# Optimization experiments

Measured on AMD Instinct MI355X. Metric: run time of the kernel, lower is better.

## Reference

```python
import jax, jax.numpy as jnp
import numpy as np

P = 16  # patch size

def _transpose_mask(w, h):
    # torch loop: skip transpose iff j > W/3 and j < 2W/3 and k > H/3 and k < 2H/3
    jj = np.arange(w)
    kk = np.arange(h)
    inner_j = (jj > w / 3) & (jj < 2 * w / 3)
    inner_k = (kk > h / 3) & (kk < 2 * h / 3)
    keep = inner_j[:, None] & inner_k[None, :]        # (w, h) inner region, unchanged
    return jnp.asarray(~keep)                          # True -> transpose patch

def setup_inputs() -> dict:
    key = jax.random.key(0)
    x = jax.random.normal(key, (256, 3, 224, 224), dtype=jnp.float32)
    return {"x": x}

def reference(x):
    B, C, Hi, Wi = x.shape
    h, w = Hi // P, Wi // P
    # 'b c (h p1) (w p2) -> b w h p1 p2 c'
    xp = x.reshape(B, C, h, P, w, P).transpose(0, 4, 2, 3, 5, 1)  # (B, w, h, p1, p2, C)
    mask = _transpose_mask(w, h)                                    # (w, h)
    xt = jnp.swapaxes(xp, 3, 4)                                     # per-patch p1<->p2 transpose
    xo = jnp.where(mask[None, :, :, None, None, None], xt, xp)
    # 'b w h p2 p1 c -> b c (h p2) (w p1)'
    out = xo.transpose(0, 5, 2, 3, 1, 4).reshape(B, C, h * P, w * P)
    return out
```

## Files before the change

kernel.cpp:

```cpp
#include <hip/hip_runtime.h>


constexpr int PS = 16;
constexpr int LP = 17;

__global__ __launch_bounds__(256) void patch_rot_kernel(
    const float* __restrict__ in, float* __restrict__ out,
    int h, int w, int Wi) {
  __shared__ float lds[4][PS * LP];

  const int wave = threadIdx.x >> 6;
  const int lane = threadIdx.x & 63;
  const int pid  = blockIdx.x * 4 + wave;

  const int wj = pid % w;
  const int t1 = pid / w;
  const int hk = t1 % h;
  const int bc = t1 / h;

  const long plane = (long)bc * (long)(h * PS) * (long)Wi;

  const int i  = lane >> 2;
  const int j4 = (lane & 3) << 2;

  const long off = plane + (long)(hk * PS + i) * Wi + (long)(wj * PS + j4);

  const float4 v = *reinterpret_cast<const float4*>(in + off);

  const bool inner = (3 * wj > w) && (3 * wj < 2 * w) &&
                     (3 * hk > h) && (3 * hk < 2 * h);

  float* L = lds[wave];
  L[i * LP + j4 + 0] = v.x;
  L[i * LP + j4 + 1] = v.y;
  L[i * LP + j4 + 2] = v.z;
  L[i * LP + j4 + 3] = v.w;
  __syncthreads();

  float4 o;
  if (!inner) {
    o.x = L[(j4 + 0) * LP + i];
    o.y = L[(j4 + 1) * LP + i];
    o.z = L[(j4 + 2) * LP + i];
    o.w = L[(j4 + 3) * LP + i];
  } else {
    o = v;
  }

  *reinterpret_cast<float4*>(out + off) = o;
}

extern "C" void kernel_launch(void* const* d_in, const int* in_sizes, int n_in,
                              void* d_out, int out_size, void* d_ws, size_t ws_size,
                              hipStream_t stream) {
  const float* in = (const float*)d_in[0];
  float* out = (float*)d_out;

  const int B = 256, C = 3, Hi = 224, Wi = 224;
  const int h = Hi / PS;
  const int w = Wi / PS;

  const int npatch = B * C * h * w;
  const int nblocks = npatch / 4;

  patch_rot_kernel<<<nblocks, 256, 0, stream>>>(in, out, h, w, Wi);
}
```

Baseline: 58.30 us.

## Process four patches per wave and replace block barrier with LDS waitcnt

Measured after the change: 67.08 us. 1.15x slower.

```diff
diff --git a/kernel.cpp b/kernel.cpp
--- a/kernel.cpp
+++ b/kernel.cpp
@@ -1,53 +1,69 @@
 #include <hip/hip_runtime.h>
 
 
-constexpr int PS = 16;
-constexpr int LP = 17;
+constexpr int PS  = 16;
+constexpr int LP  = 17;
+constexpr int PPW = 4;
 
 __global__ __launch_bounds__(256) void patch_rot_kernel(
     const float* __restrict__ in, float* __restrict__ out,
     int h, int w, int Wi) {
-  __shared__ float lds[4][PS * LP];
+  __shared__ float lds[4][PPW][PS * LP];
 
-  const int wave = threadIdx.x >> 6;
-  const int lane = threadIdx.x & 63;
-  const int pid  = blockIdx.x * 4 + wave;
-
-  const int wj = pid % w;
-  const int t1 = pid / w;
-  const int hk = t1 % h;
-  const int bc = t1 / h;
-
-  const long plane = (long)bc * (long)(h * PS) * (long)Wi;
+  const int wave  = threadIdx.x >> 6;
+  const int lane  = threadIdx.x & 63;
+  const int pbase = (blockIdx.x * 4 + wave) * PPW;
 
   const int i  = lane >> 2;
   const int j4 = (lane & 3) << 2;
 
-  const long off = plane + (long)(hk * PS + i) * Wi + (long)(wj * PS + j4);
+  long   off[PPW];
+  bool   inner[PPW];
+  float4 v[PPW];
 
-  const float4 v = *reinterpret_cast<const float4*>(in + off);
+#pragma unroll
+  for (int p = 0; p < PPW; ++p) {
+    const int pid = pbase + p;
+    const int wj  = pid % w;
+    const int t1  = pid / w;
+    const int hk  = t1 % h;
+    const int bc  = t1 / h;
 
-  const bool inner = (3 * wj > w) && (3 * wj < 2 * w) &&
-                     (3 * hk > h) && (3 * hk < 2 * h);
+    off[p] = (long)bc * (long)(h * PS) * (long)Wi
+           + (long)(hk * PS + i) * Wi
+           + (long)(wj * PS + j4);
 
-  float* L = lds[wave];
-  L[i * LP + j4 + 0] = v.x;
-  L[i * LP + j4 + 1] = v.y;
-  L[i * LP + j4 + 2] = v.z;
-  L[i * LP + j4 + 3] = v.w;
-  __syncthreads();
+    inner[p] = (3 * wj > w) && (3 * wj < 2 * w) &&
+               (3 * hk > h) && (3 * hk < 2 * h);
 
-  float4 o;
-  if (!inner) {
-    o.x = L[(j4 + 0) * LP + i];
-    o.y = L[(j4 + 1) * LP + i];
-    o.z = L[(j4 + 2) * LP + i];
-    o.w = L[(j4 + 3) * LP + i];
-  } else {
-    o = v;
+    v[p] = *reinterpret_cast<const float4*>(in + off[p]);
   }
 
-  *reinterpret_cast<float4*>(out + off) = o;
+#pragma unroll
+  for (int p = 0; p < PPW; ++p) {
+    float* L = lds[wave][p];
+    L[i * LP + j4 + 0] = v[p].x;
+    L[i * LP + j4 + 1] = v[p].y;
+    L[i * LP + j4 + 2] = v[p].z;
+    L[i * LP + j4 + 3] = v[p].w;
+  }
+
+  asm volatile("s_waitcnt lgkmcnt(0)" ::: "memory");
+
+#pragma unroll
+  for (int p = 0; p < PPW; ++p) {
+    float4 o;
+    if (!inner[p]) {
+      const float* L = lds[wave][p];
+      o.x = L[(j4 + 0) * LP + i];
+      o.y = L[(j4 + 1) * LP + i];
+      o.z = L[(j4 + 2) * LP + i];
+      o.w = L[(j4 + 3) * LP + i];
+    } else {
+      o = v[p];
+    }
+    *reinterpret_cast<float4*>(out + off[p]) = o;
+  }
 }
 
 extern "C" void kernel_launch(void* const* d_in, const int* in_sizes, int n_in,
@@ -60,8 +76,8 @@
   const int h = Hi / PS;
   const int w = Wi / PS;
 
-  const int npatch = B * C * h * w;
-  const int nblocks = npatch / 4;
+  const int npatch  = B * C * h * w;
+  const int nblocks = npatch / (4 * PPW);
 
   patch_rot_kernel<<<nblocks, 256, 0, stream>>>(in, out, h, w, Wi);
 }
```

## Transpose patches in registers with 4x4 per-thread blocks instead of LDS

Applied to the files above, without the earlier changes.

Result: faster. 54.45 us (-6.6%).

```diff
diff --git a/kernel.cpp b/kernel.cpp
--- a/kernel.cpp
+++ b/kernel.cpp
@@ -2,52 +2,57 @@
 
 
 constexpr int PS = 16;
-constexpr int LP = 17;
+
+__device__ __forceinline__ float pick(const float4& f, int m) {
+  return m == 0 ? f.x : m == 1 ? f.y : m == 2 ? f.z : f.w;
+}
 
 __global__ __launch_bounds__(256) void patch_rot_kernel(
     const float* __restrict__ in, float* __restrict__ out,
     int h, int w, int Wi) {
-  __shared__ float lds[4][PS * LP];
+  const int tid  = threadIdx.x;
+  const int t16  = tid & 15;
+  const int pid  = blockIdx.x * 16 + (tid >> 4);
 
-  const int wave = threadIdx.x >> 6;
-  const int lane = threadIdx.x & 63;
-  const int pid  = blockIdx.x * 4 + wave;
+  const int r = t16 & 3;
+  const int c = t16 >> 2;
 
   const int wj = pid % w;
   const int t1 = pid / w;
   const int hk = t1 % h;
   const int bc = t1 / h;
 
-  const long plane = (long)bc * (long)(h * PS) * (long)Wi;
-
-  const int i  = lane >> 2;
-  const int j4 = (lane & 3) << 2;
-
-  const long off = plane + (long)(hk * PS + i) * Wi + (long)(wj * PS + j4);
-
-  const float4 v = *reinterpret_cast<const float4*>(in + off);
+  const long base = (long)bc * (long)(h * PS) * (long)Wi
+                  + (long)(hk * PS) * (long)Wi
+                  + (long)(wj * PS);
 
   const bool inner = (3 * wj > w) && (3 * wj < 2 * w) &&
                      (3 * hk > h) && (3 * hk < 2 * h);
 
-  float* L = lds[wave];
-  L[i * LP + j4 + 0] = v.x;
-  L[i * LP + j4 + 1] = v.y;
-  L[i * LP + j4 + 2] = v.z;
-  L[i * LP + j4 + 3] = v.w;
-  __syncthreads();
+  const int lrow0 = inner ? 4 * r : 4 * c;
+  const int lcol  = inner ? 4 * c : 4 * r;
 
-  float4 o;
-  if (!inner) {
-    o.x = L[(j4 + 0) * LP + i];
-    o.y = L[(j4 + 1) * LP + i];
-    o.z = L[(j4 + 2) * LP + i];
-    o.w = L[(j4 + 3) * LP + i];
-  } else {
-    o = v;
+  float4 v[4];
+#pragma unroll
+  for (int k = 0; k < 4; ++k) {
+    v[k] = *reinterpret_cast<const float4*>(
+        in + base + (long)(lrow0 + k) * Wi + lcol);
   }
 
-  *reinterpret_cast<float4*>(out + off) = o;
+#pragma unroll
+  for (int m = 0; m < 4; ++m) {
+    float4 o;
+    if (inner) {
+      o = v[m];
+    } else {
+      o.x = pick(v[0], m);
+      o.y = pick(v[1], m);
+      o.z = pick(v[2], m);
+      o.w = pick(v[3], m);
+    }
+    *reinterpret_cast<float4*>(
+        out + base + (long)(4 * r + m) * Wi + 4 * c) = o;
+  }
 }
 
 extern "C" void kernel_launch(void* const* d_in, const int* in_sizes, int n_in,
@@ -60,8 +65,8 @@
   const int h = Hi / PS;
   const int w = Wi / PS;
 
-  const int npatch = B * C * h * w;
-  const int nblocks = npatch / 4;
+  const int npatch  = B * C * h * w;
+  const int nblocks = npatch / 16;
 
   patch_rot_kernel<<<nblocks, 256, 0, stream>>>(in, out, h, w, Wi);
 }
```
